# Performance work log

Hardware: AMD Instinct MI355X
Metric: run time of the kernel (lower is better)

Reference implementation:

```python
import jax, jax.numpy as jnp
import numpy as np

N_NODES = 500000
F_DIM = 256
T = 16
L0 = 65536  # layer-0 nodeset size (batch * T)
L1 = 4096   # minibatch size
SLOPE = 0.01  # torch F.leaky_relu default negative_slope


def _pinsage_conv(h, nodeset, nb_nodes, nb_w, Qw, Qb, Ww, Wb):
    # gather self and neighbor embeddings
    h_self = h[nodeset]                                   # (n, F)
    h_nb = h[nb_nodes]                                    # (n, T, F)
    h_nb = jax.nn.leaky_relu(h_nb @ Qw.T + Qb, SLOPE)     # Linear Q + leaky relu
    denom = nb_w.sum(axis=1, keepdims=True)
    denom = jnp.where(denom == 0, jnp.ones_like(denom), denom)  # safediv
    h_agg = jnp.einsum('nt,ntf->nf', nb_w, h_nb) / denom  # weighted mean
    h_cat = jnp.concatenate([h_self, h_agg], axis=1)      # (n, 2F)
    h_new = jax.nn.leaky_relu(h_cat @ Ww.T + Wb, SLOPE)   # Linear W + leaky relu
    nrm = jnp.linalg.norm(h_new, axis=1, keepdims=True)
    nrm = jnp.where(nrm == 0, jnp.ones_like(nrm), nrm)    # safediv
    return h_new / nrm


def setup_inputs() -> dict:
    key = jax.random.key(0)
    ks = jax.random.split(key, 16)
    s = 1.0 / np.sqrt(F_DIM)
    return {
        'h': jax.random.normal(ks[0], (N_NODES, F_DIM), jnp.float32),
        'Q0_w': jax.random.normal(ks[1], (F_DIM, F_DIM), jnp.float32) * s,
        'Q0_b': jnp.zeros((F_DIM,), jnp.float32),
        'W0_w': jax.random.normal(ks[2], (F_DIM, 2 * F_DIM), jnp.float32) * s,
        'W0_b': jnp.zeros((F_DIM,), jnp.float32),
        'Q1_w': jax.random.normal(ks[3], (F_DIM, F_DIM), jnp.float32) * s,
        'Q1_b': jnp.zeros((F_DIM,), jnp.float32),
        'W1_w': jax.random.normal(ks[4], (F_DIM, 2 * F_DIM), jnp.float32) * s,
        'W1_b': jnp.zeros((F_DIM,), jnp.float32),
        'nb_weights0': jax.random.uniform(ks[5], (L0, T), jnp.float32),
        'nb_weights1': jax.random.uniform(ks[6], (L1, T), jnp.float32),
        'nodeset0': jax.random.randint(ks[7], (L0,), 0, N_NODES, jnp.int32).astype(jnp.int64) if False else jax.random.randint(ks[7], (L0,), 0, N_NODES),
        'nb_nodes0': jax.random.randint(ks[8], (L0, T), 0, N_NODES),
        'nodeset1': jax.random.randint(ks[9], (L1,), 0, N_NODES),
        'nb_nodes1': jax.random.randint(ks[10], (L1, T), 0, N_NODES),
    }


def reference(h, Q0_w, Q0_b, W0_w, W0_b, Q1_w, Q1_b, W1_w, W1_b,
              nb_weights0, nb_weights1, nodeset0, nb_nodes0, nodeset1, nb_nodes1):
    # layer 0: compute new embeddings for the expanded nodeset and scatter back
    new0 = _pinsage_conv(h, nodeset0, nb_nodes0, nb_weights0, Q0_w, Q0_b, W0_w, W0_b)
    h = h.at[nodeset0].set(new0)
    # layer 1: minibatch nodeset, reads the updated table
    new1 = _pinsage_conv(h, nodeset1, nb_nodes1, nb_weights1, Q1_w, Q1_b, W1_w, W1_b)
    h = h.at[nodeset1].set(new1)
    return h[nodeset1]
```

## Files before the change

### kernel.cpp

```cpp
#include <hip/hip_runtime.h>

#define F 256
#define TNB 16
#define SLOPE 0.01f

typedef __attribute__((ext_vector_type(8))) short short8;
typedef __attribute__((ext_vector_type(4))) short short4v;
typedef __attribute__((ext_vector_type(4))) float f32x4;

__device__ __forceinline__ short f2b(float f) {
    unsigned u = __builtin_bit_cast(unsigned, f);
    u = (u + 0x7FFFu + ((u >> 16) & 1u)) >> 16;
    return (short)u;
}
__device__ __forceinline__ float b2f(short s) {
    return __builtin_bit_cast(float, ((unsigned)(unsigned short)s) << 16);
}
__device__ __forceinline__ void gld_lds16(const void* g, void* l) {
    __builtin_amdgcn_global_load_lds((const __attribute__((address_space(1))) void*)g,
                                     (__attribute__((address_space(3))) void*)l, 16, 0, 0);
}

__global__ void init_map_kernel(int* __restrict__ map, int n) {
    int i = blockIdx.x * blockDim.x + threadIdx.x;
    if (i < n) map[i] = -1;
}
__global__ void build_map_kernel(int* __restrict__ map, const int* __restrict__ nodeset, int n) {
    int i = blockIdx.x * blockDim.x + threadIdx.x;
    if (i < n) atomicMax(&map[nodeset[i]], i);
}
__global__ void cvt_bf16_kernel(const float* __restrict__ src, short* __restrict__ dst, int n) {
    int i = blockIdx.x * blockDim.x + threadIdx.x;
    if (i < n) dst[i] = f2b(src[i]);
}

__global__ __launch_bounds__(256, 2) void qh_kernel(
    const float* __restrict__ h,
    const float* __restrict__ Qw, const float* __restrict__ Qb,
    short* __restrict__ qh, int NTILES)
{
    __shared__ __align__(16) float Abuf[2][16][256];

    const int tid  = threadIdx.x;
    const int wave = tid >> 6;
    const int lane = tid & 63;
    const int brow = lane & 15;
    const int kgrp = lane >> 4;
    const int slice = wave;

    short8 bq[8][4];
    #pragma unroll
    for (int kk = 0; kk < 8; ++kk)
        #pragma unroll
        for (int ni = 0; ni < 4; ++ni) {
            const float* bp = Qw + ((size_t)(slice * 64 + ni * 16 + brow)) * 256
                                 + kk * 32 + kgrp * 8;
            float4 u0 = *(const float4*)(bp);
            float4 u1 = *(const float4*)(bp + 4);
            short8 s;
            s[0] = f2b(u0.x); s[1] = f2b(u0.y); s[2] = f2b(u0.z); s[3] = f2b(u0.w);
            s[4] = f2b(u1.x); s[5] = f2b(u1.y); s[6] = f2b(u1.z); s[7] = f2b(u1.w);
            bq[kk][ni] = s;
        }
    float qb[4];
    #pragma unroll
    for (int ni = 0; ni < 4; ++ni) qb[ni] = Qb[slice * 64 + ni * 16 + brow];
    asm volatile("" ::: "memory");

    auto stage = [&](int b, int t) {
        #pragma unroll
        for (int i = 0; i < 4; ++i) {
            int r = wave * 4 + i;
            const char* src = (const char*)(h + (((size_t)(t * 16 + r)) << 8))
                              + (((lane & ~7) | ((lane ^ r) & 7)) << 4);
            gld_lds16(src, (char*)&Abuf[b][r][0]);
        }
    };

    int t = blockIdx.x;
    const int stride = gridDim.x;
    if (t >= NTILES) return;

    stage(0, t);
    __syncthreads();
    int cur = 0;

    while (t < NTILES) {
        const int tn = t + stride;
        if (tn < NTILES) stage(cur ^ 1, tn);

        f32x4 acc[4];
        #pragma unroll
        for (int ni = 0; ni < 4; ++ni) acc[ni] = (f32x4)0.f;

        #pragma unroll
        for (int kk = 0; kk < 8; ++kk) {
            const int g0 = kk * 8 + kgrp * 2;
            const int g1 = g0 + 1;
            const float* rowp = &Abuf[cur][brow][0];
            float4 u0 = *(const float4*)(rowp + (((g0 & ~7) | ((g0 ^ brow) & 7)) << 2));
            float4 u1 = *(const float4*)(rowp + (((g1 & ~7) | ((g1 ^ brow) & 7)) << 2));
            short8 a;
            a[0] = f2b(u0.x); a[1] = f2b(u0.y); a[2] = f2b(u0.z); a[3] = f2b(u0.w);
            a[4] = f2b(u1.x); a[5] = f2b(u1.y); a[6] = f2b(u1.z); a[7] = f2b(u1.w);
            #pragma unroll
            for (int ni = 0; ni < 4; ++ni)
                acc[ni] = __builtin_amdgcn_mfma_f32_16x16x32_bf16(a, bq[kk][ni], acc[ni], 0, 0, 0);
        }

        const int row0 = t * 16 + kgrp * 4;
        #pragma unroll
        for (int ni = 0; ni < 4; ++ni) {
            #pragma unroll
            for (int r = 0; r < 4; ++r) {
                float v = acc[ni][r] + qb[ni];
                v = fmaxf(v, SLOPE * v);
                qh[(((size_t)(row0 + r)) << 8) + slice * 64 + ni * 16 + brow] = f2b(v);
            }
        }

        __syncthreads();
        cur ^= 1;
        t = tn;
    }
}

__global__ __launch_bounds__(256, 4) void agg_kernel(
    const short* __restrict__ qh, const int* __restrict__ nb_nodes,
    const float* __restrict__ nb_w, short* __restrict__ agg)
{
    const int wave = threadIdx.x >> 6;
    const int lane = threadIdx.x & 63;
    const int n = blockIdx.x * 4 + wave;

    int idx = nb_nodes[n * 16 + (lane & 15)];
    float wt = nb_w[n * 16 + (lane & 15)];
    float denom = wt;
    #pragma unroll
    for (int m = 1; m < 16; m <<= 1) denom += __shfl_xor(denom, m, 64);
    if (denom == 0.f) denom = 1.f;
    const float inv_d = 1.0f / denom;

    float a0 = 0.f, a1 = 0.f, a2 = 0.f, a3 = 0.f;
    #pragma unroll
    for (int t = 0; t < 16; ++t) {
        int g = __shfl(idx, t, 64);
        float w = __shfl(wt, t, 64);
        short4v v = *((const short4v*)(qh + ((size_t)g << 8)) + lane);
        a0 = fmaf(w, b2f(v.x), a0);
        a1 = fmaf(w, b2f(v.y), a1);
        a2 = fmaf(w, b2f(v.z), a2);
        a3 = fmaf(w, b2f(v.w), a3);
    }
    short4v o;
    o.x = f2b(a0 * inv_d); o.y = f2b(a1 * inv_d);
    o.z = f2b(a2 * inv_d); o.w = f2b(a3 * inv_d);
    *((short4v*)(agg + ((size_t)n << 8)) + lane) = o;
}

__global__ __launch_bounds__(256, 4) void w0_kernel(
    const float* __restrict__ h, const short* __restrict__ agg,
    const int* __restrict__ nodeset,
    const short* __restrict__ Wwb, const float* __restrict__ Wb,
    short* __restrict__ new0)
{
    __shared__ __align__(16) short Acat[32][512];
    __shared__ float nsq_sh[32];

    const int tid  = threadIdx.x;
    const int wave = tid >> 6;
    const int lane = tid & 63;
    const int brow = lane & 15;
    const int kgrp = lane >> 4;
    const int base = blockIdx.x * 32;

    if (tid < 32) nsq_sh[tid] = 0.f;

    float wb[4];
    #pragma unroll
    for (int ni = 0; ni < 4; ++ni) wb[ni] = Wb[wave * 64 + ni * 16 + brow];

    #pragma unroll
    for (int i = 0; i < 8; ++i) {
        int r = wave * 8 + i;
        int node = base + r;
        int g = nodeset[node];
        float4 vf = *((const float4*)(h + ((size_t)g << 8)) + lane);
        short4v s; s.x = f2b(vf.x); s.y = f2b(vf.y); s.z = f2b(vf.z); s.w = f2b(vf.w);
        short4v a = *((const short4v*)(agg + ((size_t)node << 8)) + lane);
        int gx = lane >> 1;
        char* rb = (char*)&Acat[0][0] + r * 1024;
        *(short4v*)(rb + (((gx & ~7) | ((gx ^ r) & 7)) << 4) + ((lane & 1) << 3)) = s;
        int gx2 = 32 + gx;
        *(short4v*)(rb + (((gx2 & ~7) | ((gx2 ^ r) & 7)) << 4) + ((lane & 1) << 3)) = a;
    }
    __syncthreads();

    f32x4 acc[2][4];
    #pragma unroll
    for (int mi = 0; mi < 2; ++mi)
        #pragma unroll
        for (int ni = 0; ni < 4; ++ni) acc[mi][ni] = (f32x4)0.f;

    #pragma unroll
    for (int kk = 0; kk < 16; ++kk) {
        const int gx = kk * 4 + kgrp;
        short8 a[2];
        #pragma unroll
        for (int mi = 0; mi < 2; ++mi) {
            int arow = mi * 16 + brow;
            a[mi] = *(const short8*)((const char*)&Acat[0][0] + arow * 1024 +
                                     (((gx & ~7) | ((gx ^ arow) & 7)) << 4));
        }
        #pragma unroll
        for (int ni = 0; ni < 4; ++ni) {
            short8 b = *(const short8*)(
                Wwb + (((size_t)(wave * 64 + ni * 16 + brow)) << 9) + kk * 32 + kgrp * 8);
            #pragma unroll
            for (int mi = 0; mi < 2; ++mi)
                acc[mi][ni] = __builtin_amdgcn_mfma_f32_16x16x32_bf16(a[mi], b, acc[mi][ni], 0, 0, 0);
        }
    }

    float vv[2][4][4];
    float ps[2][4];
    #pragma unroll
    for (int mi = 0; mi < 2; ++mi)
        #pragma unroll
        for (int r = 0; r < 4; ++r) ps[mi][r] = 0.f;
    #pragma unroll
    for (int mi = 0; mi < 2; ++mi)
        #pragma unroll
        for (int ni = 0; ni < 4; ++ni)
            #pragma unroll
            for (int r = 0; r < 4; ++r) {
                float v = acc[mi][ni][r] + wb[ni];
                v = fmaxf(v, SLOPE * v);
                vv[mi][ni][r] = v;
                ps[mi][r] = fmaf(v, v, ps[mi][r]);
            }
    #pragma unroll
    for (int m = 1; m < 16; m <<= 1)
        #pragma unroll
        for (int mi = 0; mi < 2; ++mi)
            #pragma unroll
            for (int r = 0; r < 4; ++r) ps[mi][r] += __shfl_xor(ps[mi][r], m, 64);
    if (brow == 0) {
        #pragma unroll
        for (int mi = 0; mi < 2; ++mi)
            #pragma unroll
            for (int r = 0; r < 4; ++r)
                atomicAdd(&nsq_sh[mi * 16 + kgrp * 4 + r], ps[mi][r]);
    }
    __syncthreads();

    #pragma unroll
    for (int mi = 0; mi < 2; ++mi)
        #pragma unroll
        for (int r = 0; r < 4; ++r) {
            int row = mi * 16 + kgrp * 4 + r;
            float nrm = sqrtf(nsq_sh[row]);
            if (nrm == 0.f) nrm = 1.f;
            float inv_n = 1.0f / nrm;
            #pragma unroll
            for (int ni = 0; ni < 4; ++ni)
                new0[((size_t)(base + row) << 8) + wave * 64 + ni * 16 + brow] =
                    f2b(vv[mi][ni][r] * inv_n);
        }
}

__device__ __forceinline__ short8 load_row16(const float* __restrict__ h,
                                             const short* __restrict__ new0,
                                             const int* __restrict__ map0,
                                             int g, int gx) {
    int m = map0[g];
    if (m >= 0)
        return *(const short8*)((const char*)new0 + (((size_t)m) << 9) + (gx << 4));
    const float* p = h + (((size_t)g) << 8) + gx * 8;
    float4 u0 = *(const float4*)p;
    float4 u1 = *(const float4*)(p + 4);
    short8 s;
    s[0] = f2b(u0.x); s[1] = f2b(u0.y); s[2] = f2b(u0.z); s[3] = f2b(u0.w);
    s[4] = f2b(u1.x); s[5] = f2b(u1.y); s[6] = f2b(u1.z); s[7] = f2b(u1.w);
    return s;
}

__global__ __launch_bounds__(256, 2) void conv_mfma_kernel(
    const float* __restrict__ h, const short* __restrict__ new0,
    const int* __restrict__ map0,
    const int* __restrict__ nodeset, const int* __restrict__ nb_nodes,
    const float* __restrict__ nb_w,
    const short* __restrict__ Qwb, const float* __restrict__ Qb,
    const short* __restrict__ Wwb, const float* __restrict__ Wb,
    float* __restrict__ out)
{
    __shared__ __align__(16) short Abuf[2][32][256];
    __shared__ __align__(16) short Hself[16][256];
    __shared__ __align__(16) short Hagg[16][264];
    __shared__ float wsh[16][16];
    __shared__ float nsq_sh[16];

    const int tid  = threadIdx.x;
    const int wave = tid >> 6;
    const int lane = tid & 63;
    const int brow = lane & 15;
    const int kgrp = lane >> 4;
    const int nb_base = blockIdx.x * 16;

    wsh[tid >> 4][tid & 15] = nb_w[nb_base * TNB + tid];
    if (tid < 16) nsq_sh[tid] = 0.f;

    float qb[4], wb[4];
    #pragma unroll
    for (int ni = 0; ni < 4; ++ni) {
        qb[ni] = Qb[wave * 64 + ni * 16 + brow];
        wb[ni] = Wb[wave * 64 + ni * 16 + brow];
    }

    const int rl = wave * 8 + (lane >> 3);
    const int sb = lane & 7;
    auto rowgid = [&](int rnd) {
        int nl = rnd * 2 + (rl >> 4);
        return nb_nodes[(nb_base + nl) * TNB + (rl & 15)];
    };

    {
        const int rl2  = wave * 4 + (lane >> 4);
        const int slot = lane & 15;
        int gs = nodeset[nb_base + rl2];
        short8 s0 = load_row16(h, new0, map0, gs, slot);
        short8 s1 = load_row16(h, new0, map0, gs, slot + 16);
        char* dstS = (char*)&Hself[0][0] + rl2 * 512 + ((slot ^ (rl2 & 7)) << 4);
        *(short8*)(dstS)       = s0;
        *(short8*)(dstS + 256) = s1;
    }
    {
        int gA = rowgid(0);
        short8 v0 = load_row16(h, new0, map0, gA, sb);
        short8 v1 = load_row16(h, new0, map0, gA, sb + 8);
        short8 v2 = load_row16(h, new0, map0, gA, sb + 16);
        short8 v3 = load_row16(h, new0, map0, gA, sb + 24);
        char* dstA = (char*)&Abuf[0][0][0] + rl * 512 + ((sb ^ (rl & 7)) << 4);
        *(short8*)(dstA)       = v0;
        *(short8*)(dstA + 128) = v1;
        *(short8*)(dstA + 256) = v2;
        *(short8*)(dstA + 384) = v3;
    }
    int gCur = rowgid(1);

    short8 bq[8][4];
    #pragma unroll
    for (int kk = 0; kk < 8; ++kk)
        #pragma unroll
        for (int ni = 0; ni < 4; ++ni)
            bq[kk][ni] = *(const short8*)(
                Qwb + (((size_t)(wave * 64 + ni * 16 + brow)) << 8) + kk * 32 + kgrp * 8);

    __syncthreads();

    #pragma unroll
    for (int rnd = 0; rnd < 8; ++rnd) {
        const int b = rnd & 1;
        int gNext = 0;
        if (rnd < 6) gNext = rowgid(rnd + 2);
        short8 w0, w1, w2, w3;
        if (rnd < 7) {
            w0 = load_row16(h, new0, map0, gCur, sb);
            w1 = load_row16(h, new0, map0, gCur, sb + 8);
            w2 = load_row16(h, new0, map0, gCur, sb + 16);
            w3 = load_row16(h, new0, map0, gCur, sb + 24);
        }

        const char* ab = (const char*)&Abuf[b][0][0];
        f32x4 acc[2][4];
        #pragma unroll
        for (int mi = 0; mi < 2; ++mi)
            #pragma unroll
            for (int ni = 0; ni < 4; ++ni) acc[mi][ni] = (f32x4)0.f;

        #pragma unroll
        for (int kk = 0; kk < 8; ++kk) {
            const int sx = ((kk * 4 + kgrp) ^ (brow & 7)) << 4;
            short8 a0 = *(const short8*)(ab + brow * 512 + sx);
            short8 a1 = *(const short8*)(ab + (16 + brow) * 512 + sx);
            #pragma unroll
            for (int ni = 0; ni < 4; ++ni) {
                acc[0][ni] = __builtin_amdgcn_mfma_f32_16x16x32_bf16(a0, bq[kk][ni], acc[0][ni], 0, 0, 0);
                acc[1][ni] = __builtin_amdgcn_mfma_f32_16x16x32_bf16(a1, bq[kk][ni], acc[1][ni], 0, 0, 0);
            }
        }

        #pragma unroll
        for (int mi = 0; mi < 2; ++mi) {
            const int nl = rnd * 2 + mi;
            float denom = 0.f;
            #pragma unroll
            for (int t = 0; t < TNB; ++t) denom += wsh[nl][t];
            if (denom == 0.f) denom = 1.f;
            float inv_d = 1.0f / denom;
            float w4[4];
            #pragma unroll
            for (int r = 0; r < 4; ++r) w4[r] = wsh[nl][kgrp * 4 + r];
            #pragma unroll
            for (int ni = 0; ni < 4; ++ni) {
                float pacc = 0.f;
                #pragma unroll
                for (int r = 0; r < 4; ++r) {
                    float v = acc[mi][ni][r] + qb[ni];
                    v = fmaxf(v, SLOPE * v);
                    pacc = fmaf(w4[r], v, pacc);
                }
                pacc += __shfl_xor(pacc, 16, 64);
                pacc += __shfl_xor(pacc, 32, 64);
                if (kgrp == 0) Hagg[nl][wave * 64 + ni * 16 + brow] = f2b(pacc * inv_d);
            }
        }

        if (rnd < 7) {
            char* dstA = (char*)&Abuf[b ^ 1][0][0] + rl * 512 + ((sb ^ (rl & 7)) << 4);
            *(short8*)(dstA)       = w0;
            *(short8*)(dstA + 128) = w1;
            *(short8*)(dstA + 256) = w2;
            *(short8*)(dstA + 384) = w3;
            gCur = gNext;
        }
        __syncthreads();
    }

    f32x4 acc2[4];
    #pragma unroll
    for (int ni = 0; ni < 4; ++ni) acc2[ni] = (f32x4)0.f;

    #pragma unroll
    for (int kk = 0; kk < 8; ++kk) {
        const int sx = ((kk * 4 + kgrp) ^ (brow & 7)) << 4;
        short8 a = *(const short8*)((const char*)&Hself[0][0] + brow * 512 + sx);
        #pragma unroll
        for (int ni = 0; ni < 4; ++ni) {
            short8 bb = *(const short8*)(
                Wwb + (((size_t)(wave * 64 + ni * 16 + brow)) << 9) + kk * 32 + kgrp * 8);
            acc2[ni] = __builtin_amdgcn_mfma_f32_16x16x32_bf16(a, bb, acc2[ni], 0, 0, 0);
        }
    }
    #pragma unroll
    for (int kk = 0; kk < 8; ++kk) {
        short8 a = *(const short8*)(&Hagg[brow][kk * 32 + kgrp * 8]);
        #pragma unroll
        for (int ni = 0; ni < 4; ++ni) {
            short8 bb = *(const short8*)(
                Wwb + (((size_t)(wave * 64 + ni * 16 + brow)) << 9) + 256 + kk * 32 + kgrp * 8);
            acc2[ni] = __builtin_amdgcn_mfma_f32_16x16x32_bf16(a, bb, acc2[ni], 0, 0, 0);
        }
    }

    float vv[4][4];
    float ps[4] = {0.f, 0.f, 0.f, 0.f};
    #pragma unroll
    for (int ni = 0; ni < 4; ++ni)
        #pragma unroll
        for (int r = 0; r < 4; ++r) {
            float v = acc2[ni][r] + wb[ni];
            v = fmaxf(v, SLOPE * v);
            vv[ni][r] = v;
            ps[r] = fmaf(v, v, ps[r]);
        }
    #pragma unroll
    for (int m = 1; m < 16; m <<= 1)
        #pragma unroll
        for (int r = 0; r < 4; ++r) ps[r] += __shfl_xor(ps[r], m, 64);
    if (brow == 0) {
        #pragma unroll
        for (int r = 0; r < 4; ++r) atomicAdd(&nsq_sh[kgrp * 4 + r], ps[r]);
    }
    __syncthreads();

    #pragma unroll
    for (int r = 0; r < 4; ++r) {
        int node = kgrp * 4 + r;
        float nrm = sqrtf(nsq_sh[node]);
        if (nrm == 0.f) nrm = 1.f;
        float inv_n = 1.0f / nrm;
        #pragma unroll
        for (int ni = 0; ni < 4; ++ni)
            out[(size_t)(nb_base + node) * F + wave * 64 + ni * 16 + brow] = vv[ni][r] * inv_n;
    }
}

__global__ void gather_out_kernel(float* __restrict__ out, const float* __restrict__ new1,
                                  const int* __restrict__ map1, const int* __restrict__ nodeset1) {
    int i = blockIdx.x;
    int f = threadIdx.x;
    int w = map1[nodeset1[i]];
    out[(size_t)i * F + f] = new1[(size_t)w * F + f];
}

extern "C" void kernel_launch(void* const* d_in, const int* in_sizes, int n_in,
                              void* d_out, int out_size, void* d_ws, size_t ws_size,
                              hipStream_t stream) {
    const float* h    = (const float*)d_in[0];
    const float* Q0w  = (const float*)d_in[1];
    const float* Q0b  = (const float*)d_in[2];
    const float* W0w  = (const float*)d_in[3];
    const float* W0b  = (const float*)d_in[4];
    const float* Q1w  = (const float*)d_in[5];
    const float* Q1b  = (const float*)d_in[6];
    const float* W1w  = (const float*)d_in[7];
    const float* W1b  = (const float*)d_in[8];
    const float* nbw0 = (const float*)d_in[9];
    const float* nbw1 = (const float*)d_in[10];
    const int* ns0    = (const int*)d_in[11];
    const int* nbn0   = (const int*)d_in[12];
    const int* ns1    = (const int*)d_in[13];
    const int* nbn1   = (const int*)d_in[14];

    const int L0 = in_sizes[11];
    const int L1 = in_sizes[13];
    const int NN = in_sizes[0] / F;

    char* ws = (char*)d_ws;
    short* qh   = (short*)ws; ws += (size_t)NN * F * sizeof(short);
    short* agg  = (short*)ws; ws += (size_t)L0 * F * sizeof(short);
    int* map0 = (int*)ws;     ws += (size_t)NN * sizeof(int);
    int* map1 = (int*)ws;     ws += (size_t)NN * sizeof(int);
    short* W0wb = (short*)ws; ws += (size_t)F * 2 * F * sizeof(short);
    short* Q1wb = (short*)ws; ws += (size_t)F * F * sizeof(short);
    short* W1wb = (short*)ws;
    short* new0 = qh;
    float* new1 = (float*)((char*)qh + ((size_t)48 << 20));

    cvt_bf16_kernel<<<(F * 2 * F + 255) / 256, 256, 0, stream>>>(W0w, W0wb, F * 2 * F);
    cvt_bf16_kernel<<<(F * F + 255) / 256, 256, 0, stream>>>(Q1w, Q1wb, F * F);
    cvt_bf16_kernel<<<(F * 2 * F + 255) / 256, 256, 0, stream>>>(W1w, W1wb, F * 2 * F);
    init_map_kernel<<<(NN + 255) / 256, 256, 0, stream>>>(map0, NN);
    init_map_kernel<<<(NN + 255) / 256, 256, 0, stream>>>(map1, NN);
    build_map_kernel<<<(L0 + 255) / 256, 256, 0, stream>>>(map0, ns0, L0);
    build_map_kernel<<<(L1 + 255) / 256, 256, 0, stream>>>(map1, ns1, L1);

    const int NTILES = NN / 16;
    qh_kernel<<<512, 256, 0, stream>>>(h, Q0w, Q0b, qh, NTILES);
    agg_kernel<<<L0 / 4, 256, 0, stream>>>(qh, nbn0, nbw0, agg);
    w0_kernel<<<L0 / 32, 256, 0, stream>>>(h, agg, ns0, W0wb, W0b, new0);

    conv_mfma_kernel<<<L1 / 16, 256, 0, stream>>>(
        h, new0, map0, ns1, nbn1, nbw1, Q1wb, Q1b, W1wb, W1b, new1);
    gather_out_kernel<<<L1, 256, 0, stream>>>((float*)d_out, new1, map1, ns1);
}
```

Baseline: 400.9 us.

## Fuse neighbor aggregation into W0 kernel and double qh tile rows

Removes the separate aggregation kernel: the W0 kernel now gathers the 16 neighbor rows of qh and computes the weighted mean directly while building its LDS tile, so the agg buffer no longer makes a round trip through global memory. The qh projection kernel also processes 32-row tiles instead of 16, reusing each register-held weight fragment across two MFMA row blocks. Workspace layout is reorganized so new0 and new1 get dedicated buffers rather than aliasing qh. In exchange, the W0 kernel takes on the latency-bound gather work with less parallelism per node. The qh kernel uses twice the LDS for its double buffer, which may affect occupancy.

```diff
diff --git a/kernel.cpp b/kernel.cpp
--- a/kernel.cpp
+++ b/kernel.cpp
@@ -39,11 +39,10 @@
     const float* __restrict__ Qw, const float* __restrict__ Qb,
     short* __restrict__ qh, int NTILES)
 {
-    __shared__ __align__(16) float Abuf[2][16][256];
-
-    const int tid  = threadIdx.x;
-    const int wave = tid >> 6;
-    const int lane = tid & 63;
+    __shared__ __align__(16) float Abuf[2][32][256];
+
+    const int lane = threadIdx.x & 63;
+    const int wave = threadIdx.x >> 6;
     const int brow = lane & 15;
     const int kgrp = lane >> 4;
     const int slice = wave;
@@ -69,9 +68,9 @@
 
     auto stage = [&](int b, int t) {
         #pragma unroll
-        for (int i = 0; i < 4; ++i) {
-            int r = wave * 4 + i;
-            const char* src = (const char*)(h + (((size_t)(t * 16 + r)) << 8))
+        for (int i = 0; i < 8; ++i) {
+            int r = wave * 8 + i;
+            const char* src = (const char*)(h + (((size_t)(t * 32 + r)) << 8))
                               + (((lane & ~7) | ((lane ^ r) & 7)) << 4);
             gld_lds16(src, (char*)&Abuf[b][r][0]);
         }
@@ -89,33 +88,42 @@
         const int tn = t + stride;
         if (tn < NTILES) stage(cur ^ 1, tn);
 
-        f32x4 acc[4];
-        #pragma unroll
-        for (int ni = 0; ni < 4; ++ni) acc[ni] = (f32x4)0.f;
+        f32x4 acc[2][4];
+        #pragma unroll
+        for (int mi = 0; mi < 2; ++mi)
+            #pragma unroll
+            for (int ni = 0; ni < 4; ++ni) acc[mi][ni] = (f32x4)0.f;
 
         #pragma unroll
         for (int kk = 0; kk < 8; ++kk) {
             const int g0 = kk * 8 + kgrp * 2;
             const int g1 = g0 + 1;
-            const float* rowp = &Abuf[cur][brow][0];
-            float4 u0 = *(const float4*)(rowp + (((g0 & ~7) | ((g0 ^ brow) & 7)) << 2));
-            float4 u1 = *(const float4*)(rowp + (((g1 & ~7) | ((g1 ^ brow) & 7)) << 2));
-            short8 a;
-            a[0] = f2b(u0.x); a[1] = f2b(u0.y); a[2] = f2b(u0.z); a[3] = f2b(u0.w);
-            a[4] = f2b(u1.x); a[5] = f2b(u1.y); a[6] = f2b(u1.z); a[7] = f2b(u1.w);
-            #pragma unroll
-            for (int ni = 0; ni < 4; ++ni)
-                acc[ni] = __builtin_amdgcn_mfma_f32_16x16x32_bf16(a, bq[kk][ni], acc[ni], 0, 0, 0);
-        }
-
-        const int row0 = t * 16 + kgrp * 4;
-        #pragma unroll
-        for (int ni = 0; ni < 4; ++ni) {
-            #pragma unroll
-            for (int r = 0; r < 4; ++r) {
-                float v = acc[ni][r] + qb[ni];
-                v = fmaxf(v, SLOPE * v);
-                qh[(((size_t)(row0 + r)) << 8) + slice * 64 + ni * 16 + brow] = f2b(v);
+            #pragma unroll
+            for (int mi = 0; mi < 2; ++mi) {
+                const int row = mi * 16 + brow;
+                const float* rowp = &Abuf[cur][row][0];
+                float4 u0 = *(const float4*)(rowp + (((g0 & ~7) | ((g0 ^ row) & 7)) << 2));
+                float4 u1 = *(const float4*)(rowp + (((g1 & ~7) | ((g1 ^ row) & 7)) << 2));
+                short8 a;
+                a[0] = f2b(u0.x); a[1] = f2b(u0.y); a[2] = f2b(u0.z); a[3] = f2b(u0.w);
+                a[4] = f2b(u1.x); a[5] = f2b(u1.y); a[6] = f2b(u1.z); a[7] = f2b(u1.w);
+                #pragma unroll
+                for (int ni = 0; ni < 4; ++ni)
+                    acc[mi][ni] = __builtin_amdgcn_mfma_f32_16x16x32_bf16(a, bq[kk][ni], acc[mi][ni], 0, 0, 0);
+            }
+        }
+
+        #pragma unroll
+        for (int mi = 0; mi < 2; ++mi) {
+            const int row0 = t * 32 + mi * 16 + kgrp * 4;
+            #pragma unroll
+            for (int ni = 0; ni < 4; ++ni) {
+                #pragma unroll
+                for (int r = 0; r < 4; ++r) {
+                    float v = acc[mi][ni][r] + qb[ni];
+                    v = fmaxf(v, SLOPE * v);
+                    qh[(((size_t)(row0 + r)) << 8) + slice * 64 + ni * 16 + brow] = f2b(v);
+                }
             }
         }
 
@@ -125,42 +133,10 @@
     }
 }
 
-__global__ __launch_bounds__(256, 4) void agg_kernel(
-    const short* __restrict__ qh, const int* __restrict__ nb_nodes,
-    const float* __restrict__ nb_w, short* __restrict__ agg)
-{
-    const int wave = threadIdx.x >> 6;
-    const int lane = threadIdx.x & 63;
-    const int n = blockIdx.x * 4 + wave;
-
-    int idx = nb_nodes[n * 16 + (lane & 15)];
-    float wt = nb_w[n * 16 + (lane & 15)];
-    float denom = wt;
-    #pragma unroll
-    for (int m = 1; m < 16; m <<= 1) denom += __shfl_xor(denom, m, 64);
-    if (denom == 0.f) denom = 1.f;
-    const float inv_d = 1.0f / denom;
-
-    float a0 = 0.f, a1 = 0.f, a2 = 0.f, a3 = 0.f;
-    #pragma unroll
-    for (int t = 0; t < 16; ++t) {
-        int g = __shfl(idx, t, 64);
-        float w = __shfl(wt, t, 64);
-        short4v v = *((const short4v*)(qh + ((size_t)g << 8)) + lane);
-        a0 = fmaf(w, b2f(v.x), a0);
-        a1 = fmaf(w, b2f(v.y), a1);
-        a2 = fmaf(w, b2f(v.z), a2);
-        a3 = fmaf(w, b2f(v.w), a3);
-    }
-    short4v o;
-    o.x = f2b(a0 * inv_d); o.y = f2b(a1 * inv_d);
-    o.z = f2b(a2 * inv_d); o.w = f2b(a3 * inv_d);
-    *((short4v*)(agg + ((size_t)n << 8)) + lane) = o;
-}
-
 __global__ __launch_bounds__(256, 4) void w0_kernel(
-    const float* __restrict__ h, const short* __restrict__ agg,
+    const float* __restrict__ h, const short* __restrict__ qh,
     const int* __restrict__ nodeset,
+    const int* __restrict__ nb_nodes, const float* __restrict__ nb_w,
     const short* __restrict__ Wwb, const float* __restrict__ Wb,
     short* __restrict__ new0)
 {
@@ -184,15 +160,39 @@
     for (int i = 0; i < 8; ++i) {
         int r = wave * 8 + i;
         int node = base + r;
+
         int g = nodeset[node];
         float4 vf = *((const float4*)(h + ((size_t)g << 8)) + lane);
         short4v s; s.x = f2b(vf.x); s.y = f2b(vf.y); s.z = f2b(vf.z); s.w = f2b(vf.w);
-        short4v a = *((const short4v*)(agg + ((size_t)node << 8)) + lane);
+
+        int idx  = nb_nodes[node * 16 + (lane & 15)];
+        float wt = nb_w[node * 16 + (lane & 15)];
+        float denom = wt;
+        #pragma unroll
+        for (int m = 1; m < 16; m <<= 1) denom += __shfl_xor(denom, m, 64);
+        if (denom == 0.f) denom = 1.f;
+        const float inv_d = 1.0f / denom;
+
+        float a0 = 0.f, a1 = 0.f, a2 = 0.f, a3 = 0.f;
+        #pragma unroll
+        for (int t = 0; t < 16; ++t) {
+            int gg = __shfl(idx, t, 64);
+            float w = __shfl(wt, t, 64);
+            short4v v = *((const short4v*)(qh + ((size_t)gg << 8)) + lane);
+            a0 = fmaf(w, b2f(v.x), a0);
+            a1 = fmaf(w, b2f(v.y), a1);
+            a2 = fmaf(w, b2f(v.z), a2);
+            a3 = fmaf(w, b2f(v.w), a3);
+        }
+        short4v o;
+        o.x = f2b(a0 * inv_d); o.y = f2b(a1 * inv_d);
+        o.z = f2b(a2 * inv_d); o.w = f2b(a3 * inv_d);
+
         int gx = lane >> 1;
         char* rb = (char*)&Acat[0][0] + r * 1024;
         *(short4v*)(rb + (((gx & ~7) | ((gx ^ r) & 7)) << 4) + ((lane & 1) << 3)) = s;
         int gx2 = 32 + gx;
-        *(short4v*)(rb + (((gx2 & ~7) | ((gx2 ^ r) & 7)) << 4) + ((lane & 1) << 3)) = a;
+        *(short4v*)(rb + (((gx2 & ~7) | ((gx2 ^ r) & 7)) << 4) + ((lane & 1) << 3)) = o;
     }
     __syncthreads();
 
@@ -519,14 +519,13 @@
 
     char* ws = (char*)d_ws;
     short* qh   = (short*)ws; ws += (size_t)NN * F * sizeof(short);
-    short* agg  = (short*)ws; ws += (size_t)L0 * F * sizeof(short);
+    short* new0 = (short*)ws; ws += (size_t)L0 * F * sizeof(short);
+    float* new1 = (float*)ws; ws += (size_t)L1 * F * sizeof(float);
     int* map0 = (int*)ws;     ws += (size_t)NN * sizeof(int);
     int* map1 = (int*)ws;     ws += (size_t)NN * sizeof(int);
     short* W0wb = (short*)ws; ws += (size_t)F * 2 * F * sizeof(short);
     short* Q1wb = (short*)ws; ws += (size_t)F * F * sizeof(short);
     short* W1wb = (short*)ws;
-    short* new0 = qh;
-    float* new1 = (float*)((char*)qh + ((size_t)48 << 20));
 
     cvt_bf16_kernel<<<(F * 2 * F + 255) / 256, 256, 0, stream>>>(W0w, W0wb, F * 2 * F);
     cvt_bf16_kernel<<<(F * F + 255) / 256, 256, 0, stream>>>(Q1w, Q1wb, F * F);
@@ -536,10 +535,9 @@
     build_map_kernel<<<(L0 + 255) / 256, 256, 0, stream>>>(map0, ns0, L0);
     build_map_kernel<<<(L1 + 255) / 256, 256, 0, stream>>>(map1, ns1, L1);
 
-    const int NTILES = NN / 16;
+    const int NTILES = NN / 32;
     qh_kernel<<<512, 256, 0, stream>>>(h, Q0w, Q0b, qh, NTILES);
-    agg_kernel<<<L0 / 4, 256, 0, stream>>>(qh, nbn0, nbw0, agg);
-    w0_kernel<<<L0 / 32, 256, 0, stream>>>(h, agg, ns0, W0wb, W0b, new0);
+    w0_kernel<<<L0 / 32, 256, 0, stream>>>(h, qh, ns0, nbn0, nbw0, W0wb, W0b, new0);
 
     conv_mfma_kernel<<<L1 / 16, 256, 0, stream>>>(
         h, new0, map0, ns1, nbn1, nbw1, Q1wb, Q1b, W1wb, W1b, new1);
```

After: 409.7 us. +2.2%, slower.
